# Optimization experiments

Measured on AMD Instinct MI355X. Metric: run time of the kernel, lower is better.

## Reference

```python
import jax, jax.numpy as jnp
import numpy as np


def setup_inputs() -> dict:
    key = jax.random.key(0)
    B, S, I, H, O = 32, 2048, 128, 512, 128
    ks = jax.random.split(key, 24)
    sc = 0.05
    d = {
        "x": jax.random.normal(ks[0], (B, S, I), jnp.float32),
        "h0": jnp.zeros((B, 2, H), jnp.float32),
        "l0_wxz": jax.random.normal(ks[1], (H, I)) * sc,
        "l0_bxz": jax.random.normal(ks[2], (H,)) * sc,
        "l0_whz": jax.random.normal(ks[3], (H, H)) * sc,
        "l0_wxr": jax.random.normal(ks[4], (H, I)) * sc,
        "l0_bxr": jax.random.normal(ks[5], (H,)) * sc,
        "l0_whr": jax.random.normal(ks[6], (H, H)) * sc,
        "l0_wxg": jax.random.normal(ks[7], (H, I)) * sc,
        "l0_bxg": jax.random.normal(ks[8], (H,)) * sc,
        "l0_whg": jax.random.normal(ks[9], (H, H)) * sc,
        "l1_wxz": jax.random.normal(ks[10], (H, H)) * sc,
        "l1_bxz": jax.random.normal(ks[11], (H,)) * sc,
        "l1_whz": jax.random.normal(ks[12], (H, H)) * sc,
        "l1_wxr": jax.random.normal(ks[13], (H, H)) * sc,
        "l1_bxr": jax.random.normal(ks[14], (H,)) * sc,
        "l1_whr": jax.random.normal(ks[15], (H, H)) * sc,
        "l1_wxg": jax.random.normal(ks[16], (H, H)) * sc,
        "l1_bxg": jax.random.normal(ks[17], (H,)) * sc,
        "l1_whg": jax.random.normal(ks[18], (H, H)) * sc,
        "wy": jax.random.normal(ks[19], (O, H)) * sc,
        "by": jax.random.normal(ks[20], (O,)) * sc,
    }
    return d


def _gru_cell(xt, h, wxz, bxz, whz, wxr, bxr, whr, wxg, bxg, whg):
    # z = sigmoid(Wxz x + bxz + Whz h); r = sigmoid(...); g = tanh(Wxg x + bxg + Whg (r*h))
    z = jax.nn.sigmoid(xt @ wxz.T + bxz + h @ whz.T)
    r = jax.nn.sigmoid(xt @ wxr.T + bxr + h @ whr.T)
    g = jnp.tanh(xt @ wxg.T + bxg + (r * h) @ whg.T)
    return z * h + (1.0 - z) * g


def reference(x, h0,
              l0_wxz, l0_bxz, l0_whz, l0_wxr, l0_bxr, l0_whr, l0_wxg, l0_bxg, l0_whg,
              l1_wxz, l1_bxz, l1_whz, l1_wxr, l1_bxr, l1_whr, l1_wxg, l1_bxg, l1_whg,
              wy, by):
    p0 = (l0_wxz, l0_bxz, l0_whz, l0_wxr, l0_bxr, l0_whr, l0_wxg, l0_bxg, l0_whg)
    p1 = (l1_wxz, l1_bxz, l1_whz, l1_wxr, l1_bxr, l1_whr, l1_wxg, l1_bxg, l1_whg)

    def step(carry, xt):  # xt: (B, I)
        h0_, h1_ = carry
        h0n = _gru_cell(xt, h0_, *p0)
        h1n = _gru_cell(h0n, h1_, *p1)
        y = h1n @ wy.T + by
        return (h0n, h1n), y

    xs = jnp.swapaxes(x, 0, 1)  # (S, B, I)
    init = (h0[:, 0, :], h0[:, 1, :])
    (hf0, hf1), ys = jax.lax.scan(step, init, xs)
    layer_output = jnp.swapaxes(ys, 0, 1)  # (B, S, O)
    hidden_state = jnp.stack([hf0, hf1], axis=1)  # (B, L, H)
    return layer_output, hidden_state
```

## Files before the change

### kernel.cpp

```cpp
#include <hip/hip_runtime.h>

typedef __bf16 bf16x8 __attribute__((ext_vector_type(8)));
typedef float f32x4 __attribute__((ext_vector_type(4)));
typedef unsigned short u16;
typedef unsigned int u32;
typedef unsigned long long u64;

#define MFMA16(a, b, c) __builtin_amdgcn_mfma_f32_16x16x32_bf16((a), (b), (c), 0, 0, 0)

namespace {
constexpr int kB = 32, kS = 2048, kI = 128, kH = 512, kO = 128;
constexpr int NC = 2;
constexpr int BPC = 16;
constexpr int L0WG = 16;
constexpr int WGC = 48;
constexpr int NSLOT = 4;
constexpr int NT = 2 * kS + 3;
constexpr long LOUT = (long)kB * kS * kO;
constexpr u32 POISON = 0xFFFFFFFFu;

constexpr size_t WS_FLG  = 0;
constexpr size_t WS_PUB0 = 8192;
constexpr size_t BUFSZ   = (size_t)NC * NSLOT * BPC * kH * 2;
constexpr size_t WS_PUB1 = WS_PUB0 + BUFSZ;
constexpr size_t WS_PR0  = WS_PUB1 + BUFSZ;
constexpr size_t WS_PR1  = WS_PR0 + BUFSZ;
constexpr size_t WS_WTS  = WS_PR1 + BUFSZ;

constexpr int W0H = 0;
constexpr int W0X = 786432;
constexpr int W1X = 983040;
constexpr int W1H = 1769472;
constexpr int WYO = 2555904;

constexpr int CSLOT = BPC * kH;
constexpr int CBUF  = NSLOT * CSLOT;
}

__device__ __forceinline__ u16 f2bf(float f) {
  u32 x = __float_as_uint(f);
  return (u16)((x + 0x7fffu + ((x >> 16) & 1u)) >> 16);
}

__device__ __forceinline__ u64 ld64a(const u64* p) {
  return __hip_atomic_load((u64*)p, __ATOMIC_RELAXED, __HIP_MEMORY_SCOPE_AGENT);
}
__device__ __forceinline__ u32 ld32a(const u32* p) {
  return __hip_atomic_load((u32*)p, __ATOMIC_RELAXED, __HIP_MEMORY_SCOPE_AGENT);
}
__device__ __forceinline__ bool bad(u64 v) {
  return ((u32)v == POISON) | ((u32)(v >> 32) == POISON);
}

struct Frags {
  u64 v[16];
  const u64* p;
  __device__ __forceinline__ void issue(const u16* base) {
    p = (const u64*)base;
#pragma unroll
    for (int s = 0; s < 8; ++s) {
      v[2 * s]     = ld64a(p + s * 8);
      v[2 * s + 1] = ld64a(p + s * 8 + 1);
    }
  }
  __device__ __forceinline__ void settle() {
    while (true) {
      bool any = false;
#pragma unroll
      for (int i = 0; i < 16; ++i) {
        if (bad(v[i])) { any = true; v[i] = ld64a(p + (i >> 1) * 8 + (i & 1)); }
      }
      if (!any) break;
    }
  }
  __device__ __forceinline__ bf16x8 frag(int s) const {
    union { u64 d[2]; bf16x8 f; } u_;
    u_.d[0] = v[2 * s]; u_.d[1] = v[2 * s + 1];
    return u_.f;
  }
};

__device__ __forceinline__ bf16x8 pack8(float4 a, float4 b) {
  union { u16 s[8]; bf16x8 v; } u_;
  u_.s[0] = f2bf(a.x); u_.s[1] = f2bf(a.y); u_.s[2] = f2bf(a.z); u_.s[3] = f2bf(a.w);
  u_.s[4] = f2bf(b.x); u_.s[5] = f2bf(b.y); u_.s[6] = f2bf(b.z); u_.s[7] = f2bf(b.w);
  return u_.v;
}

__global__ void prep_kernel(const float* whz0, const float* whr0, const float* whg0,
                            const float* wxz0, const float* wxr0, const float* wxg0,
                            const float* wxz1, const float* wxr1, const float* wxg1,
                            const float* whz1, const float* whr1, const float* whg1,
                            const float* wy, const float* h0in, char* ws) {
  u16* wts = (u16*)(ws + WS_WTS);
  int gid = blockIdx.x * blockDim.x + threadIdx.x;
  int stride = gridDim.x * blockDim.x;
  for (int i = gid; i < 786432; i += stride) {
    int g = i >> 18, r = i & 262143;
    wts[W0H + i] = f2bf((g == 0 ? whz0 : g == 1 ? whr0 : whg0)[r]);
  }
  for (int i = gid; i < 196608; i += stride) {
    int g = i >> 16, r = i & 65535;
    wts[W0X + i] = f2bf((g == 0 ? wxz0 : g == 1 ? wxr0 : wxg0)[r]);
  }
  for (int i = gid; i < 786432; i += stride) {
    int g = i >> 18, r = i & 262143;
    wts[W1X + i] = f2bf((g == 0 ? wxz1 : g == 1 ? wxr1 : wxg1)[r]);
  }
  for (int i = gid; i < 786432; i += stride) {
    int g = i >> 18, r = i & 262143;
    wts[W1H + i] = f2bf((g == 0 ? whz1 : g == 1 ? whr1 : whg1)[r]);
  }
  for (int i = gid; i < 65536; i += stride) wts[WYO + i] = f2bf(wy[i]);

  u32* r0 = (u32*)(ws + WS_PR0);
  u32* r1 = (u32*)(ws + WS_PR1);
  u32* b0 = (u32*)(ws + WS_PUB0);
  u32* b1 = (u32*)(ws + WS_PUB1);
  constexpr int NW = (int)(BUFSZ / 4);
  for (int i = gid; i < NW; i += stride) { r0[i] = POISON; r1[i] = POISON; }
  for (int i = gid; i < NW; i += stride) {
    int s = (i >> 12) & 3;
    if (s != 3) { b0[i] = POISON; b1[i] = POISON; }
  }
  u16* p0 = (u16*)(ws + WS_PUB0);
  u16* p1 = (u16*)(ws + WS_PUB1);
  for (int i = gid; i < NC * BPC * kH; i += stride) {
    int c = i / (BPC * kH), rem = i - c * (BPC * kH);
    int b = rem / kH, k = rem - b * kH;
    int bg = c * BPC + b;
    p0[c * CBUF + 3 * CSLOT + rem] = f2bf(h0in[(size_t)bg * 2 * kH + k]);
    p1[c * CBUF + 3 * CSLOT + rem] = f2bf(h0in[(size_t)bg * 2 * kH + kH + k]);
  }
  if (gid < 2048) ((u32*)(ws + WS_FLG))[gid] = 0u;
}

__device__ __forceinline__ void st_tile(float* base, f32x4 c, int q, int li) {
#pragma unroll
  for (int r = 0; r < 4; ++r) base[(q * 4 + r) * 17 + li] = c[r];
}

__device__ __forceinline__ void pub2(u16* base, int off, float v0, float v1) {
  u32 pk = (u32)f2bf(v0) | ((u32)f2bf(v1) << 16);
  __hip_atomic_store((u32*)(base + off), pk, __ATOMIC_RELAXED, __HIP_MEMORY_SCOPE_AGENT);
}
__device__ __forceinline__ void poison2(u16* base, int off) {
  __hip_atomic_store((u32*)(base + off), POISON, __ATOMIC_RELAXED, __HIP_MEMORY_SCOPE_AGENT);
}

__device__ __forceinline__ float sigm(float x) { return 1.f / (1.f + __expf(-x)); }
__device__ __forceinline__ float tanh_f(float x) {
  float te = __expf(-2.f * fabsf(x));
  return __builtin_copysignf((1.f - te) / (1.f + te), x);
}

__global__ __launch_bounds__(256, 1)
void gru_kernel(const float* __restrict__ xg, const float* __restrict__ h0in,
                const float* __restrict__ bxz0, const float* __restrict__ bxr0,
                const float* __restrict__ bxg0, const float* __restrict__ bxz1,
                const float* __restrict__ bxr1, const float* __restrict__ bxg1,
                const float* __restrict__ byv, float* __restrict__ out, char* ws) {
  const int cl = blockIdx.x / WGC;
  const int wid = blockIdx.x - cl * WGC;
  const bool isL0 = wid < L0WG;
  const int w0 = wid, w1 = wid - L0WG;
  const int tid = threadIdx.x;
  const int lane = tid & 63, wv = tid >> 6;
  const int q = lane >> 4, li = lane & 15;
  const int kh = wv & 1;
  const int nt = wv >> 1;
  const bool xside = wv < 2;

  u16* pub0 = (u16*)(ws + WS_PUB0) + (size_t)cl * CBUF;
  u16* pub1 = (u16*)(ws + WS_PUB1) + (size_t)cl * CBUF;
  u16* pr0  = (u16*)(ws + WS_PR0)  + (size_t)cl * CBUF;
  u16* pr1  = (u16*)(ws + WS_PR1)  + (size_t)cl * CBUF;
  const u16* wts = (const u16*)(ws + WS_WTS);
  u32* flags = (u32*)(ws + WS_FLG) + (size_t)cl * 1024;

  __shared__ __align__(16) float smem[5984];
  float* spA = smem;
  float* spB = smem;
  float* ypA = smem + 5440;

  bf16x8 wA[3][8];
  bf16x8 wE[8];
  if (isL0) {
    const int ci = w0 * 32 + nt * 16 + li;
#pragma unroll
    for (int g = 0; g < 3; ++g)
#pragma unroll
      for (int s = 0; s < 8; ++s)
        wA[g][s] = *(const bf16x8*)(wts + W0H + ((size_t)(g * kH + ci) * kH + kh * 256 + q * 8 + s * 32));
#pragma unroll
    for (int g = 0; g < 3; ++g)
#pragma unroll
      for (int s = 0; s < 2; ++s)
        wE[g * 2 + s] = *(const bf16x8*)(wts + W0X + ((size_t)(g * kH + ci) * kI + kh * 64 + q * 8 + s * 32));
  } else {
    const int ci = w1 * 16 + li;
    const int base = xside ? W1X : W1H;
#pragma unroll
    for (int g = 0; g < 3; ++g)
#pragma unroll
      for (int s = 0; s < 8; ++s)
        wA[g][s] = *(const bf16x8*)(wts + base + ((size_t)(g * kH + ci) * kH + kh * 256 + q * 8 + s * 32));
    if (!xside && w1 < 8) {
#pragma unroll
      for (int s = 0; s < 8; ++s)
        wE[s] = *(const bf16x8*)(wts + WYO + ((size_t)ci * kH + kh * 256 + q * 8 + s * 32));
    }
  }

  float2 bz2 = {0.f, 0.f}, br2 = {0.f, 0.f}, bg2 = {0.f, 0.f};
  float by_r = 0.f;
  float hm0r = 0.f, hm1r = 0.f;
  float zA0 = 0.f, zA1 = 0.f, gA0 = 0.f, gA1 = 0.f;
  if (isL0) {
    const int c0i = (tid & 15) * 2, bq = tid >> 4;
    bz2 = *(const float2*)(bxz0 + w0 * 32 + c0i);
    br2 = *(const float2*)(bxr0 + w0 * 32 + c0i);
    bg2 = *(const float2*)(bxg0 + w0 * 32 + c0i);
    const float* hp = h0in + (size_t)(cl * 16 + bq) * 2 * kH + w0 * 32 + c0i;
    hm0r = hp[0]; hm1r = hp[1];
  } else {
    const int c0i = (tid & 7) * 2, bq = tid >> 3;
    bz2 = *(const float2*)(bxz1 + w1 * 16 + c0i);
    br2 = *(const float2*)(bxr1 + w1 * 16 + c0i);
    bg2 = *(const float2*)(bxg1 + w1 * 16 + c0i);
    if (bq < 16) {
      const float* hp = h0in + (size_t)(cl * 16 + bq) * 2 * kH + kH + w1 * 16 + c0i;
      hm0r = hp[0]; hm1r = hp[1];
    }
    if (w1 < 8) by_r = byv[w1 * 16 + (tid & 15)];
  }

  for (int tk = 0; tk < NT; ++tk) {
    const bool ev = (tk & 1) == 0;
    const int t = tk >> 1;
    const int u = t - 1;
    const bool l0A = isL0 && ev && t < kS;
    const bool l0B = isL0 && !ev && t < kS;
    const bool l1A = !isL0 && ev && t >= 1 && t <= kS;
    const bool l1B = !isL0 && !ev && t >= 1 && t <= kS;
    const bool yAct = !isL0 && ev && w1 < 8 && t >= 2 && t <= kS + 1;

    u32 myfl = 0xFFFFFFFFu;
    if (lane < WGC) myfl = ld32a(flags + lane * 16);
    const u32 need = (tk >= 2) ? (u32)(tk - 2) : 0u;

    if (l0A) {
      Frags F;
      F.issue(pub0 + ((t + 3) & 3) * CSLOT + li * kH + kh * 256 + q * 8);
      const float* xr = xg + ((size_t)(cl * 16 + li) * kS + t) * kI + kh * 64 + q * 8;
      float4 xv0 = *(const float4*)xr;
      float4 xv1 = *(const float4*)(xr + 4);
      float4 xv2 = *(const float4*)(xr + 32);
      float4 xv3 = *(const float4*)(xr + 36);
      F.settle();
      f32x4 hz = {0.f, 0.f, 0.f, 0.f}, hr = hz, xz = hz, xr2 = hz, xg2 = hz;
#pragma unroll
      for (int s = 0; s < 8; ++s) {
        bf16x8 a = F.frag(s);
        hz = MFMA16(a, wA[0][s], hz);
        hr = MFMA16(a, wA[1][s], hr);
      }
      {
        bf16x8 a = pack8(xv0, xv1);
        xz  = MFMA16(a, wE[0], xz);
        xr2 = MFMA16(a, wE[2], xr2);
        xg2 = MFMA16(a, wE[4], xg2);
      }
      {
        bf16x8 a = pack8(xv2, xv3);
        xz  = MFMA16(a, wE[1], xz);
        xr2 = MFMA16(a, wE[3], xr2);
        xg2 = MFMA16(a, wE[5], xg2);
      }
      st_tile(spA + ((0 * 2 + nt) * 2 + kh) * 272, hz, q, li);
      st_tile(spA + ((1 * 2 + nt) * 2 + kh) * 272, hr, q, li);
      st_tile(spA + ((2 * 2 + nt) * 2 + kh) * 272, xz, q, li);
      st_tile(spA + ((3 * 2 + nt) * 2 + kh) * 272, xr2, q, li);
      st_tile(spA + ((4 * 2 + nt) * 2 + kh) * 272, xg2, q, li);
    } else if (!isL0 && ev) {
      if (xside) {
        if (l1A) {
          Frags F;
          F.issue(pub0 + (u & 3) * CSLOT + li * kH + kh * 256 + q * 8);
          F.settle();
          f32x4 cz = {0.f, 0.f, 0.f, 0.f}, cr = cz, cg = cz;
#pragma unroll
          for (int s = 0; s < 8; ++s) {
            bf16x8 a = F.frag(s);
            cz = MFMA16(a, wA[0][s], cz);
            cr = MFMA16(a, wA[1][s], cr);
            cg = MFMA16(a, wA[2][s], cg);
          }
          st_tile(spA + (2 * 2 + kh) * 272, cz, q, li);
          st_tile(spA + (3 * 2 + kh) * 272, cr, q, li);
          st_tile(spA + (4 * 2 + kh) * 272, cg, q, li);
        }
      } else {
        const bool rec = t >= 1 && t <= kS;
        const bool ym = (w1 < 8) && t >= 2 && t <= kS + 1;
        if (rec || ym) {
          Frags F;
          F.issue(pub1 + ((t + 2) & 3) * CSLOT + li * kH + kh * 256 + q * 8);
          F.settle();
          f32x4 cz = {0.f, 0.f, 0.f, 0.f}, cr = cz, cy = cz;
#pragma unroll
          for (int s = 0; s < 8; ++s) {
            bf16x8 a = F.frag(s);
            if (rec) {
              cz = MFMA16(a, wA[0][s], cz);
              cr = MFMA16(a, wA[1][s], cr);
            }
            if (ym) cy = MFMA16(a, wE[s], cy);
          }
          if (rec) {
            st_tile(spA + (0 * 2 + kh) * 272, cz, q, li);
            st_tile(spA + (1 * 2 + kh) * 272, cr, q, li);
          }
          if (ym) st_tile(ypA + kh * 272, cy, q, li);
        }
      }
    } else if (l0B) {
      Frags F;
      F.issue(pr0 + (t & 3) * CSLOT + li * kH + kh * 256 + q * 8);
      F.settle();
      f32x4 cg = {0.f, 0.f, 0.f, 0.f};
#pragma unroll
      for (int s = 0; s < 8; ++s) cg = MFMA16(F.frag(s), wA[2][s], cg);
      st_tile(spB + (nt * 2 + kh) * 272, cg, q, li);
    } else if (l1B && !xside) {
      Frags F;
      F.issue(pr1 + (u & 3) * CSLOT + li * kH + kh * 256 + q * 8);
      F.settle();
      f32x4 cg = {0.f, 0.f, 0.f, 0.f};
#pragma unroll
      for (int s = 0; s < 8; ++s) cg = MFMA16(F.frag(s), wA[2][s], cg);
      st_tile(spB + kh * 272, cg, q, li);
    }
    __syncthreads();

    while (__any((int)(myfl < need))) {
      if (lane < WGC) myfl = ld32a(flags + lane * 16);
    }

    if (l0A) {
      const int cp = tid & 15, b = tid >> 4;
      const int c0 = cp * 2, n2 = c0 >> 4, cc = c0 & 15, o = b * 17 + cc;
      float hz0 = spA[((0*2+n2)*2+0)*272 + o] + spA[((0*2+n2)*2+1)*272 + o];
      float hz1 = spA[((0*2+n2)*2+0)*272 + o+1] + spA[((0*2+n2)*2+1)*272 + o+1];
      float hr0 = spA[((1*2+n2)*2+0)*272 + o] + spA[((1*2+n2)*2+1)*272 + o];
      float hr1 = spA[((1*2+n2)*2+0)*272 + o+1] + spA[((1*2+n2)*2+1)*272 + o+1];
      float xz0 = spA[((2*2+n2)*2+0)*272 + o] + spA[((2*2+n2)*2+1)*272 + o];
      float xz1 = spA[((2*2+n2)*2+0)*272 + o+1] + spA[((2*2+n2)*2+1)*272 + o+1];
      float xr0 = spA[((3*2+n2)*2+0)*272 + o] + spA[((3*2+n2)*2+1)*272 + o];
      float xr1 = spA[((3*2+n2)*2+0)*272 + o+1] + spA[((3*2+n2)*2+1)*272 + o+1];
      float xg0 = spA[((4*2+n2)*2+0)*272 + o] + spA[((4*2+n2)*2+1)*272 + o];
      float xg1 = spA[((4*2+n2)*2+0)*272 + o+1] + spA[((4*2+n2)*2+1)*272 + o+1];
      zA0 = sigm(hz0 + xz0 + bz2.x);
      zA1 = sigm(hz1 + xz1 + bz2.y);
      float r0v = sigm(hr0 + xr0 + br2.x);
      float r1v = sigm(hr1 + xr1 + br2.y);
      gA0 = xg0 + bg2.x;
      gA1 = xg1 + bg2.y;
      const int off = b * kH + w0 * 32 + c0;
      pub2(pr0 + (t & 3) * CSLOT, off, r0v * hm0r, r1v * hm1r);
      poison2(pr0 + ((t + 2) & 3) * CSLOT, off);
    }
    if (l1A && tid < 128) {
      const int cp = tid & 7, b = tid >> 3;
      const int c0 = cp * 2, o = b * 17 + c0;
      float hz0 = spA[(0*2+0)*272 + o] + spA[(0*2+1)*272 + o];
      float hz1 = spA[(0*2+0)*272 + o+1] + spA[(0*2+1)*272 + o+1];
      float hr0 = spA[(1*2+0)*272 + o] + spA[(1*2+1)*272 + o];
      float hr1 = spA[(1*2+0)*272 + o+1] + spA[(1*2+1)*272 + o+1];
      float xz0 = spA[(2*2+0)*272 + o] + spA[(2*2+1)*272 + o];
      float xz1 = spA[(2*2+0)*272 + o+1] + spA[(2*2+1)*272 + o+1];
      float xr0 = spA[(3*2+0)*272 + o] + spA[(3*2+1)*272 + o];
      float xr1 = spA[(3*2+0)*272 + o+1] + spA[(3*2+1)*272 + o+1];
      float xg0 = spA[(4*2+0)*272 + o] + spA[(4*2+1)*272 + o];
      float xg1 = spA[(4*2+0)*272 + o+1] + spA[(4*2+1)*272 + o+1];
      zA0 = sigm(hz0 + xz0 + bz2.x);
      zA1 = sigm(hz1 + xz1 + bz2.y);
      float r0v = sigm(hr0 + xr0 + br2.x);
      float r1v = sigm(hr1 + xr1 + br2.y);
      gA0 = xg0 + bg2.x;
      gA1 = xg1 + bg2.y;
      const int off = b * kH + w1 * 16 + c0;
      pub2(pr1 + (u & 3) * CSLOT, off, r0v * hm0r, r1v * hm1r);
      poison2(pr1 + ((u + 2) & 3) * CSLOT, off);
    }
    if (yAct) {
      const int c = tid & 15, b = tid >> 4;
      float y = ypA[b * 17 + c] + ypA[272 + b * 17 + c] + by_r;
      out[((size_t)(cl * 16 + b) * kS + (t - 2)) * kO + w1 * 16 + c] = y;
    }
    if (l0B) {
      const int cp = tid & 15, b = tid >> 4;
      const int c0 = cp * 2, n2 = c0 >> 4, cc = c0 & 15, o = b * 17 + cc;
      float gh0 = spB[(n2*2+0)*272 + o] + spB[(n2*2+1)*272 + o];
      float gh1 = spB[(n2*2+0)*272 + o+1] + spB[(n2*2+1)*272 + o+1];
      float g0 = tanh_f(gA0 + gh0), g1 = tanh_f(gA1 + gh1);
      float hn0 = zA0 * hm0r + (1.f - zA0) * g0;
      float hn1 = zA1 * hm1r + (1.f - zA1) * g1;
      hm0r = hn0; hm1r = hn1;
      const int off = b * kH + w0 * 32 + c0;
      pub2(pub0 + (t & 3) * CSLOT, off, hn0, hn1);
      poison2(pub0 + ((t + 2) & 3) * CSLOT, off);
      if (t == kS - 1) {
        float* op = out + LOUT + (size_t)(cl * 16 + b) * 2 * kH + w0 * 32 + c0;
        op[0] = hn0; op[1] = hn1;
      }
    }
    if (l1B && tid < 128) {
      const int cp = tid & 7, b = tid >> 3;
      const int c0 = cp * 2, o = b * 17 + c0;
      float gh0 = spB[0 * 272 + o] + spB[1 * 272 + o];
      float gh1 = spB[0 * 272 + o+1] + spB[1 * 272 + o+1];
      float g0 = tanh_f(gA0 + gh0), g1 = tanh_f(gA1 + gh1);
      float hn0 = zA0 * hm0r + (1.f - zA0) * g0;
      float hn1 = zA1 * hm1r + (1.f - zA1) * g1;
      hm0r = hn0; hm1r = hn1;
      const int off = b * kH + w1 * 16 + c0;
      pub2(pub1 + (u & 3) * CSLOT, off, hn0, hn1);
      poison2(pub1 + ((u + 2) & 3) * CSLOT, off);
      if (u == kS - 1) {
        float* op = out + LOUT + (size_t)(cl * 16 + b) * 2 * kH + kH + w1 * 16 + c0;
        op[0] = hn0; op[1] = hn1;
      }
    }

    __syncthreads();
    if (tid == 0 && tk != NT - 1)
      __hip_atomic_store(flags + wid * 16, (u32)(tk + 1), __ATOMIC_RELAXED,
                         __HIP_MEMORY_SCOPE_AGENT);
  }
}

extern "C" void kernel_launch(void* const* d_in, const int* in_sizes, int n_in,
                              void* d_out, int out_size, void* d_ws, size_t ws_size,
                              hipStream_t stream) {
  (void)in_sizes; (void)n_in; (void)out_size; (void)ws_size;
  const float* x      = (const float*)d_in[0];
  const float* h0     = (const float*)d_in[1];
  const float* l0_wxz = (const float*)d_in[2];
  const float* l0_bxz = (const float*)d_in[3];
  const float* l0_whz = (const float*)d_in[4];
  const float* l0_wxr = (const float*)d_in[5];
  const float* l0_bxr = (const float*)d_in[6];
  const float* l0_whr = (const float*)d_in[7];
  const float* l0_wxg = (const float*)d_in[8];
  const float* l0_bxg = (const float*)d_in[9];
  const float* l0_whg = (const float*)d_in[10];
  const float* l1_wxz = (const float*)d_in[11];
  const float* l1_bxz = (const float*)d_in[12];
  const float* l1_whz = (const float*)d_in[13];
  const float* l1_wxr = (const float*)d_in[14];
  const float* l1_bxr = (const float*)d_in[15];
  const float* l1_whr = (const float*)d_in[16];
  const float* l1_wxg = (const float*)d_in[17];
  const float* l1_bxg = (const float*)d_in[18];
  const float* l1_whg = (const float*)d_in[19];
  const float* wy     = (const float*)d_in[20];
  const float* by     = (const float*)d_in[21];
  float* out = (float*)d_out;
  char* ws = (char*)d_ws;

  prep_kernel<<<512, 256, 0, stream>>>(l0_whz, l0_whr, l0_whg, l0_wxz, l0_wxr, l0_wxg,
                                       l1_wxz, l1_wxr, l1_wxg, l1_whz, l1_whr, l1_whg,
                                       wy, h0, ws);
  gru_kernel<<<NC * WGC, 256, 0, stream>>>(x, h0, l0_bxz, l0_bxr, l0_bxg,
                                           l1_bxz, l1_bxr, l1_bxg, by, out, ws);
}
```

Before: 16.61 ms.

## Split LDS into even/odd buffers and drop trailing per-step block barrier

Gives even and odd phases separate LDS staging regions (spE/spO) and double-buffers the y-projection tile by step parity. That lets the trailing __syncthreads at the end of each step go. The mid-step barrier becomes a hand-written lgkmcnt wait plus s_barrier, and the x-side MFMAs are moved ahead of waiting on the published hidden-state fragments so their latency overlaps the spin. The aim is to cut barrier and serialization cost on the latency-bound recurrent step. The risk is that tid 0 may now raise its progress flag before other threads finish publishing, leaving correctness to the poison-based settle mechanism.

```diff
diff --git a/kernel.cpp b/kernel.cpp
--- a/kernel.cpp
+++ b/kernel.cpp
@@ -50,6 +50,15 @@
 }
 __device__ __forceinline__ bool bad(u64 v) {
   return ((u32)v == POISON) | ((u32)(v >> 32) == POISON);
+}
+
+__device__ __forceinline__ void bar_lgkm() {
+  __builtin_amdgcn_sched_barrier(0);
+  asm volatile("s_waitcnt lgkmcnt(0)" ::: "memory");
+  __builtin_amdgcn_sched_barrier(0);
+  __builtin_amdgcn_s_barrier();
+  __builtin_amdgcn_sched_barrier(0);
+  asm volatile("" ::: "memory");
 }
 
 struct Frags {
@@ -178,10 +187,10 @@
   const u16* wts = (const u16*)(ws + WS_WTS);
   u32* flags = (u32*)(ws + WS_FLG) + (size_t)cl * 1024;
 
-  __shared__ __align__(16) float smem[5984];
-  float* spA = smem;
-  float* spB = smem;
-  float* ypA = smem + 5440;
+  __shared__ __align__(16) float smem[7616];
+  float* spE = smem;
+  float* spO = smem + 5440;
+  float* ypA = smem + 6528;
 
   bf16x8 wA[3][8];
   bf16x8 wE[8];
@@ -257,14 +266,7 @@
       float4 xv1 = *(const float4*)(xr + 4);
       float4 xv2 = *(const float4*)(xr + 32);
       float4 xv3 = *(const float4*)(xr + 36);
-      F.settle();
       f32x4 hz = {0.f, 0.f, 0.f, 0.f}, hr = hz, xz = hz, xr2 = hz, xg2 = hz;
-#pragma unroll
-      for (int s = 0; s < 8; ++s) {
-        bf16x8 a = F.frag(s);
-        hz = MFMA16(a, wA[0][s], hz);
-        hr = MFMA16(a, wA[1][s], hr);
-      }
       {
         bf16x8 a = pack8(xv0, xv1);
         xz  = MFMA16(a, wE[0], xz);
@@ -277,11 +279,18 @@
         xr2 = MFMA16(a, wE[3], xr2);
         xg2 = MFMA16(a, wE[5], xg2);
       }
-      st_tile(spA + ((0 * 2 + nt) * 2 + kh) * 272, hz, q, li);
-      st_tile(spA + ((1 * 2 + nt) * 2 + kh) * 272, hr, q, li);
-      st_tile(spA + ((2 * 2 + nt) * 2 + kh) * 272, xz, q, li);
-      st_tile(spA + ((3 * 2 + nt) * 2 + kh) * 272, xr2, q, li);
-      st_tile(spA + ((4 * 2 + nt) * 2 + kh) * 272, xg2, q, li);
+      F.settle();
+#pragma unroll
+      for (int s = 0; s < 8; ++s) {
+        bf16x8 a = F.frag(s);
+        hz = MFMA16(a, wA[0][s], hz);
+        hr = MFMA16(a, wA[1][s], hr);
+      }
+      st_tile(spE + ((0 * 2 + nt) * 2 + kh) * 272, hz, q, li);
+      st_tile(spE + ((1 * 2 + nt) * 2 + kh) * 272, hr, q, li);
+      st_tile(spE + ((2 * 2 + nt) * 2 + kh) * 272, xz, q, li);
+      st_tile(spE + ((3 * 2 + nt) * 2 + kh) * 272, xr2, q, li);
+      st_tile(spE + ((4 * 2 + nt) * 2 + kh) * 272, xg2, q, li);
     } else if (!isL0 && ev) {
       if (xside) {
         if (l1A) {
@@ -296,9 +305,9 @@
             cr = MFMA16(a, wA[1][s], cr);
             cg = MFMA16(a, wA[2][s], cg);
           }
-          st_tile(spA + (2 * 2 + kh) * 272, cz, q, li);
-          st_tile(spA + (3 * 2 + kh) * 272, cr, q, li);
-          st_tile(spA + (4 * 2 + kh) * 272, cg, q, li);
+          st_tile(spE + (2 * 2 + kh) * 272, cz, q, li);
+          st_tile(spE + (3 * 2 + kh) * 272, cr, q, li);
+          st_tile(spE + (4 * 2 + kh) * 272, cg, q, li);
         }
       } else {
         const bool rec = t >= 1 && t <= kS;
@@ -318,10 +327,10 @@
             if (ym) cy = MFMA16(a, wE[s], cy);
           }
           if (rec) {
-            st_tile(spA + (0 * 2 + kh) * 272, cz, q, li);
-            st_tile(spA + (1 * 2 + kh) * 272, cr, q, li);
+            st_tile(spE + (0 * 2 + kh) * 272, cz, q, li);
+            st_tile(spE + (1 * 2 + kh) * 272, cr, q, li);
           }
-          if (ym) st_tile(ypA + kh * 272, cy, q, li);
+          if (ym) st_tile(ypA + (t & 1) * 544 + kh * 272, cy, q, li);
         }
       }
     } else if (l0B) {
@@ -331,7 +340,7 @@
       f32x4 cg = {0.f, 0.f, 0.f, 0.f};
 #pragma unroll
       for (int s = 0; s < 8; ++s) cg = MFMA16(F.frag(s), wA[2][s], cg);
-      st_tile(spB + (nt * 2 + kh) * 272, cg, q, li);
+      st_tile(spO + (nt * 2 + kh) * 272, cg, q, li);
     } else if (l1B && !xside) {
       Frags F;
       F.issue(pr1 + (u & 3) * CSLOT + li * kH + kh * 256 + q * 8);
@@ -339,9 +348,10 @@
       f32x4 cg = {0.f, 0.f, 0.f, 0.f};
 #pragma unroll
       for (int s = 0; s < 8; ++s) cg = MFMA16(F.frag(s), wA[2][s], cg);
-      st_tile(spB + kh * 272, cg, q, li);
-    }
-    __syncthreads();
+      st_tile(spO + kh * 272, cg, q, li);
+    }
+
+    bar_lgkm();
 
     while (__any((int)(myfl < need))) {
       if (lane < WGC) myfl = ld32a(flags + lane * 16);
@@ -350,16 +360,16 @@
     if (l0A) {
       const int cp = tid & 15, b = tid >> 4;
       const int c0 = cp * 2, n2 = c0 >> 4, cc = c0 & 15, o = b * 17 + cc;
-      float hz0 = spA[((0*2+n2)*2+0)*272 + o] + spA[((0*2+n2)*2+1)*272 + o];
-      float hz1 = spA[((0*2+n2)*2+0)*272 + o+1] + spA[((0*2+n2)*2+1)*272 + o+1];
-      float hr0 = spA[((1*2+n2)*2+0)*272 + o] + spA[((1*2+n2)*2+1)*272 + o];
-      float hr1 = spA[((1*2+n2)*2+0)*272 + o+1] + spA[((1*2+n2)*2+1)*272 + o+1];
-      float xz0 = spA[((2*2+n2)*2+0)*272 + o] + spA[((2*2+n2)*2+1)*272 + o];
-      float xz1 = spA[((2*2+n2)*2+0)*272 + o+1] + spA[((2*2+n2)*2+1)*272 + o+1];
-      float xr0 = spA[((3*2+n2)*2+0)*272 + o] + spA[((3*2+n2)*2+1)*272 + o];
-      float xr1 = spA[((3*2+n2)*2+0)*272 + o+1] + spA[((3*2+n2)*2+1)*272 + o+1];
-      float xg0 = spA[((4*2+n2)*2+0)*272 + o] + spA[((4*2+n2)*2+1)*272 + o];
-      float xg1 = spA[((4*2+n2)*2+0)*272 + o+1] + spA[((4*2+n2)*2+1)*272 + o+1];
+      float hz0 = spE[((0*2+n2)*2+0)*272 + o] + spE[((0*2+n2)*2+1)*272 + o];
+      float hz1 = spE[((0*2+n2)*2+0)*272 + o+1] + spE[((0*2+n2)*2+1)*272 + o+1];
+      float hr0 = spE[((1*2+n2)*2+0)*272 + o] + spE[((1*2+n2)*2+1)*272 + o];
+      float hr1 = spE[((1*2+n2)*2+0)*272 + o+1] + spE[((1*2+n2)*2+1)*272 + o+1];
+      float xz0 = spE[((2*2+n2)*2+0)*272 + o] + spE[((2*2+n2)*2+1)*272 + o];
+      float xz1 = spE[((2*2+n2)*2+0)*272 + o+1] + spE[((2*2+n2)*2+1)*272 + o+1];
+      float xr0 = spE[((3*2+n2)*2+0)*272 + o] + spE[((3*2+n2)*2+1)*272 + o];
+      float xr1 = spE[((3*2+n2)*2+0)*272 + o+1] + spE[((3*2+n2)*2+1)*272 + o+1];
+      float xg0 = spE[((4*2+n2)*2+0)*272 + o] + spE[((4*2+n2)*2+1)*272 + o];
+      float xg1 = spE[((4*2+n2)*2+0)*272 + o+1] + spE[((4*2+n2)*2+1)*272 + o+1];
       zA0 = sigm(hz0 + xz0 + bz2.x);
       zA1 = sigm(hz1 + xz1 + bz2.y);
       float r0v = sigm(hr0 + xr0 + br2.x);
@@ -373,16 +383,16 @@
     if (l1A && tid < 128) {
       const int cp = tid & 7, b = tid >> 3;
       const int c0 = cp * 2, o = b * 17 + c0;
-      float hz0 = spA[(0*2+0)*272 + o] + spA[(0*2+1)*272 + o];
-      float hz1 = spA[(0*2+0)*272 + o+1] + spA[(0*2+1)*272 + o+1];
-      float hr0 = spA[(1*2+0)*272 + o] + spA[(1*2+1)*272 + o];
-      float hr1 = spA[(1*2+0)*272 + o+1] + spA[(1*2+1)*272 + o+1];
-      float xz0 = spA[(2*2+0)*272 + o] + spA[(2*2+1)*272 + o];
-      float xz1 = spA[(2*2+0)*272 + o+1] + spA[(2*2+1)*272 + o+1];
-      float xr0 = spA[(3*2+0)*272 + o] + spA[(3*2+1)*272 + o];
-      float xr1 = spA[(3*2+0)*272 + o+1] + spA[(3*2+1)*272 + o+1];
-      float xg0 = spA[(4*2+0)*272 + o] + spA[(4*2+1)*272 + o];
-      float xg1 = spA[(4*2+0)*272 + o+1] + spA[(4*2+1)*272 + o+1];
+      float hz0 = spE[(0*2+0)*272 + o] + spE[(0*2+1)*272 + o];
+      float hz1 = spE[(0*2+0)*272 + o+1] + spE[(0*2+1)*272 + o+1];
+      float hr0 = spE[(1*2+0)*272 + o] + spE[(1*2+1)*272 + o];
+      float hr1 = spE[(1*2+0)*272 + o+1] + spE[(1*2+1)*272 + o+1];
+      float xz0 = spE[(2*2+0)*272 + o] + spE[(2*2+1)*272 + o];
+      float xz1 = spE[(2*2+0)*272 + o+1] + spE[(2*2+1)*272 + o+1];
+      float xr0 = spE[(3*2+0)*272 + o] + spE[(3*2+1)*272 + o];
+      float xr1 = spE[(3*2+0)*272 + o+1] + spE[(3*2+1)*272 + o+1];
+      float xg0 = spE[(4*2+0)*272 + o] + spE[(4*2+1)*272 + o];
+      float xg1 = spE[(4*2+0)*272 + o+1] + spE[(4*2+1)*272 + o+1];
       zA0 = sigm(hz0 + xz0 + bz2.x);
       zA1 = sigm(hz1 + xz1 + bz2.y);
       float r0v = sigm(hr0 + xr0 + br2.x);
@@ -395,14 +405,15 @@
     }
     if (yAct) {
       const int c = tid & 15, b = tid >> 4;
-      float y = ypA[b * 17 + c] + ypA[272 + b * 17 + c] + by_r;
+      const float* yp = ypA + (t & 1) * 544;
+      float y = yp[b * 17 + c] + yp[272 + b * 17 + c] + by_r;
       out[((size_t)(cl * 16 + b) * kS + (t - 2)) * kO + w1 * 16 + c] = y;
     }
     if (l0B) {
       const int cp = tid & 15, b = tid >> 4;
       const int c0 = cp * 2, n2 = c0 >> 4, cc = c0 & 15, o = b * 17 + cc;
-      float gh0 = spB[(n2*2+0)*272 + o] + spB[(n2*2+1)*272 + o];
-      float gh1 = spB[(n2*2+0)*272 + o+1] + spB[(n2*2+1)*272 + o+1];
+      float gh0 = spO[(n2*2+0)*272 + o] + spO[(n2*2+1)*272 + o];
+      float gh1 = spO[(n2*2+0)*272 + o+1] + spO[(n2*2+1)*272 + o+1];
       float g0 = tanh_f(gA0 + gh0), g1 = tanh_f(gA1 + gh1);
       float hn0 = zA0 * hm0r + (1.f - zA0) * g0;
       float hn1 = zA1 * hm1r + (1.f - zA1) * g1;
@@ -418,8 +429,8 @@
     if (l1B && tid < 128) {
       const int cp = tid & 7, b = tid >> 3;
       const int c0 = cp * 2, o = b * 17 + c0;
-      float gh0 = spB[0 * 272 + o] + spB[1 * 272 + o];
-      float gh1 = spB[0 * 272 + o+1] + spB[1 * 272 + o+1];
+      float gh0 = spO[0 * 272 + o] + spO[1 * 272 + o];
+      float gh1 = spO[0 * 272 + o+1] + spO[1 * 272 + o+1];
       float g0 = tanh_f(gA0 + gh0), g1 = tanh_f(gA1 + gh1);
       float hn0 = zA0 * hm0r + (1.f - zA0) * g0;
       float hn1 = zA1 * hm1r + (1.f - zA1) * g1;
@@ -433,7 +444,6 @@
       }
     }
 
-    __syncthreads();
     if (tid == 0 && tk != NT - 1)
       __hip_atomic_store(flags + wid * 16, (u32)(tk + 1), __ATOMIC_RELAXED,
                          __HIP_MEMORY_SCOPE_AGENT);
```

Result: slower. 18.87 ms (+13.6%).

## Prefetch next step's hidden-state fragments and deepen publish ring to eight slots

Applied to the files above, without the earlier changes.

Each workgroup now issues the global loads for the next tick's recurrent fragments at the end of the current tick, right after signalling its flag, rather than at the start of the next tick. The publish/poison ring buffers grow from 4 to 8 slots and the flag-wait slack widens from tk-2 to tk-6. Together these let the loads overlap the cross-workgroup barrier. The layer-0 x-projection MFMAs are also moved ahead of the settle so they hide load latency. The risk is correctness: prefetched data may be read before its producer publishes, and validity then depends on the poison-and-retry protocol. The larger ring also uses more workspace.

```diff
diff --git a/kernel.cpp b/kernel.cpp
--- a/kernel.cpp
+++ b/kernel.cpp
@@ -14,7 +14,7 @@
 constexpr int BPC = 16;
 constexpr int L0WG = 16;
 constexpr int WGC = 48;
-constexpr int NSLOT = 4;
+constexpr int NSLOT = 8;
 constexpr int NT = 2 * kS + 3;
 constexpr long LOUT = (long)kB * kS * kO;
 constexpr u32 POISON = 0xFFFFFFFFu;
@@ -120,8 +120,8 @@
   constexpr int NW = (int)(BUFSZ / 4);
   for (int i = gid; i < NW; i += stride) { r0[i] = POISON; r1[i] = POISON; }
   for (int i = gid; i < NW; i += stride) {
-    int s = (i >> 12) & 3;
-    if (s != 3) { b0[i] = POISON; b1[i] = POISON; }
+    int s = (i >> 12) & 7;
+    if (s != 7) { b0[i] = POISON; b1[i] = POISON; }
   }
   u16* p0 = (u16*)(ws + WS_PUB0);
   u16* p1 = (u16*)(ws + WS_PUB1);
@@ -129,8 +129,8 @@
     int c = i / (BPC * kH), rem = i - c * (BPC * kH);
     int b = rem / kH, k = rem - b * kH;
     int bg = c * BPC + b;
-    p0[c * CBUF + 3 * CSLOT + rem] = f2bf(h0in[(size_t)bg * 2 * kH + k]);
-    p1[c * CBUF + 3 * CSLOT + rem] = f2bf(h0in[(size_t)bg * 2 * kH + kH + k]);
+    p0[c * CBUF + 7 * CSLOT + rem] = f2bf(h0in[(size_t)bg * 2 * kH + k]);
+    p1[c * CBUF + 7 * CSLOT + rem] = f2bf(h0in[(size_t)bg * 2 * kH + kH + k]);
   }
   if (gid < 2048) ((u32*)(ws + WS_FLG))[gid] = 0u;
 }
@@ -235,6 +235,34 @@
     if (w1 < 8) by_r = byv[w1 * 16 + (tid & 15)];
   }
 
+  const int foff = li * kH + kh * 256 + q * 8;
+  Frags F;
+
+  auto issue_for = [&](int tkn) {
+    const bool evn = (tkn & 1) == 0;
+    const int tn = tkn >> 1;
+    const int un = tn - 1;
+    if (isL0) {
+      if (tn < kS) {
+        if (evn) F.issue(pub0 + ((tn + 7) & 7) * CSLOT + foff);
+        else     F.issue(pr0 + (tn & 7) * CSLOT + foff);
+      }
+    } else if (xside) {
+      if (evn && tn >= 1 && tn <= kS)
+        F.issue(pub0 + (un & 7) * CSLOT + foff);
+    } else {
+      if (evn) {
+        const bool rec = tn >= 1 && tn <= kS;
+        const bool ym = (w1 < 8) && tn >= 2 && tn <= kS + 1;
+        if (rec || ym) F.issue(pub1 + ((tn + 6) & 7) * CSLOT + foff);
+      } else {
+        if (tn >= 1 && tn <= kS) F.issue(pr1 + (un & 7) * CSLOT + foff);
+      }
+    }
+  };
+
+  issue_for(0);
+
   for (int tk = 0; tk < NT; ++tk) {
     const bool ev = (tk & 1) == 0;
     const int t = tk >> 1;
@@ -247,24 +275,15 @@
 
     u32 myfl = 0xFFFFFFFFu;
     if (lane < WGC) myfl = ld32a(flags + lane * 16);
-    const u32 need = (tk >= 2) ? (u32)(tk - 2) : 0u;
+    const u32 need = (tk >= 6) ? (u32)(tk - 6) : 0u;
 
     if (l0A) {
-      Frags F;
-      F.issue(pub0 + ((t + 3) & 3) * CSLOT + li * kH + kh * 256 + q * 8);
       const float* xr = xg + ((size_t)(cl * 16 + li) * kS + t) * kI + kh * 64 + q * 8;
       float4 xv0 = *(const float4*)xr;
       float4 xv1 = *(const float4*)(xr + 4);
       float4 xv2 = *(const float4*)(xr + 32);
       float4 xv3 = *(const float4*)(xr + 36);
-      F.settle();
       f32x4 hz = {0.f, 0.f, 0.f, 0.f}, hr = hz, xz = hz, xr2 = hz, xg2 = hz;
-#pragma unroll
-      for (int s = 0; s < 8; ++s) {
-        bf16x8 a = F.frag(s);
-        hz = MFMA16(a, wA[0][s], hz);
-        hr = MFMA16(a, wA[1][s], hr);
-      }
       {
         bf16x8 a = pack8(xv0, xv1);
         xz  = MFMA16(a, wE[0], xz);
@@ -276,6 +295,13 @@
         xz  = MFMA16(a, wE[1], xz);
         xr2 = MFMA16(a, wE[3], xr2);
         xg2 = MFMA16(a, wE[5], xg2);
+      }
+      F.settle();
+#pragma unroll
+      for (int s = 0; s < 8; ++s) {
+        bf16x8 a = F.frag(s);
+        hz = MFMA16(a, wA[0][s], hz);
+        hr = MFMA16(a, wA[1][s], hr);
       }
       st_tile(spA + ((0 * 2 + nt) * 2 + kh) * 272, hz, q, li);
       st_tile(spA + ((1 * 2 + nt) * 2 + kh) * 272, hr, q, li);
@@ -285,8 +311,6 @@
     } else if (!isL0 && ev) {
       if (xside) {
         if (l1A) {
-          Frags F;
-          F.issue(pub0 + (u & 3) * CSLOT + li * kH + kh * 256 + q * 8);
           F.settle();
           f32x4 cz = {0.f, 0.f, 0.f, 0.f}, cr = cz, cg = cz;
 #pragma unroll
@@ -304,8 +328,6 @@
         const bool rec = t >= 1 && t <= kS;
         const bool ym = (w1 < 8) && t >= 2 && t <= kS + 1;
         if (rec || ym) {
-          Frags F;
-          F.issue(pub1 + ((t + 2) & 3) * CSLOT + li * kH + kh * 256 + q * 8);
           F.settle();
           f32x4 cz = {0.f, 0.f, 0.f, 0.f}, cr = cz, cy = cz;
 #pragma unroll
@@ -325,16 +347,12 @@
         }
       }
     } else if (l0B) {
-      Frags F;
-      F.issue(pr0 + (t & 3) * CSLOT + li * kH + kh * 256 + q * 8);
       F.settle();
       f32x4 cg = {0.f, 0.f, 0.f, 0.f};
 #pragma unroll
       for (int s = 0; s < 8; ++s) cg = MFMA16(F.frag(s), wA[2][s], cg);
       st_tile(spB + (nt * 2 + kh) * 272, cg, q, li);
     } else if (l1B && !xside) {
-      Frags F;
-      F.issue(pr1 + (u & 3) * CSLOT + li * kH + kh * 256 + q * 8);
       F.settle();
       f32x4 cg = {0.f, 0.f, 0.f, 0.f};
 #pragma unroll
@@ -367,8 +385,8 @@
       gA0 = xg0 + bg2.x;
       gA1 = xg1 + bg2.y;
       const int off = b * kH + w0 * 32 + c0;
-      pub2(pr0 + (t & 3) * CSLOT, off, r0v * hm0r, r1v * hm1r);
-      poison2(pr0 + ((t + 2) & 3) * CSLOT, off);
+      pub2(pr0 + (t & 7) * CSLOT, off, r0v * hm0r, r1v * hm1r);
+      poison2(pr0 + ((t + 4) & 7) * CSLOT, off);
     }
     if (l1A && tid < 128) {
       const int cp = tid & 7, b = tid >> 3;
@@ -390,8 +408,8 @@
       gA0 = xg0 + bg2.x;
       gA1 = xg1 + bg2.y;
       const int off = b * kH + w1 * 16 + c0;
-      pub2(pr1 + (u & 3) * CSLOT, off, r0v * hm0r, r1v * hm1r);
-      poison2(pr1 + ((u + 2) & 3) * CSLOT, off);
+      pub2(pr1 + (u & 7) * CSLOT, off, r0v * hm0r, r1v * hm1r);
+      poison2(pr1 + ((u + 4) & 7) * CSLOT, off);
     }
     if (yAct) {
       const int c = tid & 15, b = tid >> 4;
@@ -408,8 +426,8 @@
       float hn1 = zA1 * hm1r + (1.f - zA1) * g1;
       hm0r = hn0; hm1r = hn1;
       const int off = b * kH + w0 * 32 + c0;
-      pub2(pub0 + (t & 3) * CSLOT, off, hn0, hn1);
-      poison2(pub0 + ((t + 2) & 3) * CSLOT, off);
+      pub2(pub0 + (t & 7) * CSLOT, off, hn0, hn1);
+      poison2(pub0 + ((t + 4) & 7) * CSLOT, off);
       if (t == kS - 1) {
         float* op = out + LOUT + (size_t)(cl * 16 + b) * 2 * kH + w0 * 32 + c0;
         op[0] = hn0; op[1] = hn1;
@@ -425,8 +443,8 @@
       float hn1 = zA1 * hm1r + (1.f - zA1) * g1;
       hm0r = hn0; hm1r = hn1;
       const int off = b * kH + w1 * 16 + c0;
-      pub2(pub1 + (u & 3) * CSLOT, off, hn0, hn1);
-      poison2(pub1 + ((u + 2) & 3) * CSLOT, off);
+      pub2(pub1 + (u & 7) * CSLOT, off, hn0, hn1);
+      poison2(pub1 + ((u + 4) & 7) * CSLOT, off);
       if (u == kS - 1) {
         float* op = out + LOUT + (size_t)(cl * 16 + b) * 2 * kH + kH + w1 * 16 + c0;
         op[0] = hn0; op[1] = hn1;
@@ -437,6 +455,7 @@
     if (tid == 0 && tk != NT - 1)
       __hip_atomic_store(flags + wid * 16, (u32)(tk + 1), __ATOMIC_RELAXED,
                          __HIP_MEMORY_SCOPE_AGENT);
+    if (tk + 1 < NT) issue_for(tk + 1);
   }
 }
 
```

After: 20.85 ms. 25.6% more time.
